# Kernel tuning notes

Hardware: AMD Instinct MI355X
Metric: run time of the kernel (lower is better)

Reference implementation:

```python
import jax, jax.numpy as jnp
import numpy as np

HIDDEN = 96
N_NODES = 50000
N_EDGES = 800000
IN_DIM = 256


def setup_inputs() -> dict:
    key = jax.random.key(0)
    ks = jax.random.split(key, 8)
    x = jax.random.normal(ks[0], (N_NODES, IN_DIM), dtype=jnp.float32)
    d = jax.random.uniform(ks[1], (N_NODES,), dtype=jnp.float32)
    src = jax.random.randint(ks[2], (N_EDGES,), 0, N_NODES, dtype=jnp.int32)
    dst = jax.random.randint(ks[3], (N_EDGES,), 0, N_NODES, dtype=jnp.int32)
    # Xavier-normal-ish init scaled like the torch module (gain 1.414)
    W_in = jax.random.normal(ks[4], (HIDDEN, IN_DIM), dtype=jnp.float32) * (1.414 * np.sqrt(2.0 / (HIDDEN + IN_DIM)))
    b_in = jnp.zeros((HIDDEN,), dtype=jnp.float32)
    W_gate = jax.random.normal(ks[5], (HIDDEN, 2 * HIDDEN), dtype=jnp.float32) * (1.414 * np.sqrt(2.0 / (3 * HIDDEN)))
    b_gate = jnp.zeros((HIDDEN,), dtype=jnp.float32)
    W_clf = jax.random.normal(ks[6], (2, HIDDEN), dtype=jnp.float32) * np.sqrt(2.0 / (2 + HIDDEN))
    b_clf = jnp.zeros((2,), dtype=jnp.float32)
    return {"x": x, "d": d, "src": src, "dst": dst,
            "W_in": W_in, "b_in": b_in, "W_gate": W_gate, "b_gate": b_gate,
            "W_clf": W_clf, "b_clf": b_clf}


def reference(x, d, src, dst, W_in, b_in, W_gate, b_gate, W_clf, b_clf):
    # h = input_gate(x)
    h = x @ W_in.T + b_in                                  # [N, H]
    # NOTE: the original loop reassigns the same h every iteration, so every
    # num_layer iteration produces identical (z, a); one pass is the exact math.
    h_src = h[src]                                         # [E, H] gather
    h_dst = h[dst]                                         # [E, H] gather
    h2 = jnp.concatenate([h_dst, h_src], axis=1)           # [E, 2H]
    a = jnp.tanh((h2 @ W_gate.T + b_gate) / np.sqrt(2.0 * HIDDEN))  # [E, H]
    e = d[dst] * d[src]                                    # [E]
    msg = h_src * a * e[:, None]                           # [E, H]
    z = jax.ops.segment_sum(msg, dst, num_segments=N_NODES)  # scatter-sum to dst
    z = jax.nn.log_softmax(z @ W_clf.T + b_clf, axis=-1)   # [N, 2]
    return (z, a)
```

## Files before the change

kernel.cpp:

```cpp
#include <hip/hip_runtime.h>
#include <math.h>

#define HIDDEN 96
#define NNODES 50000
#define NEDGES 800000
#define INDIM  256
#define RS 0.07216878364870323f

__global__ void repack_kernel(const float* __restrict__ Wg, const float* __restrict__ bg,
                              float* __restrict__ V, float* __restrict__ bias2) {
    int idx = blockIdx.x * 256 + threadIdx.x;
    if (idx < 192 * 96) {
        int j = idx / 96, k = idx % 96;
        float v = (j < 96) ? Wg[j * 192 + k] : Wg[(j - 96) * 192 + 96 + k];
        V[idx] = v * RS;
    }
    if (idx < 192) bias2[idx] = (idx < 96) ? bg[idx] * RS : 0.0f;
}

__global__ __launch_bounds__(256) void gemm_nt_bias(
    const float* __restrict__ A, const float* __restrict__ B,
    const float* __restrict__ bias, float* __restrict__ C,
    int M, int K, int ldc) {
    __shared__ float As[128][36];
    __shared__ float Bs[96][36];
    const int tid = threadIdx.x;
    const int m0 = blockIdx.x * 128;
    const int n0 = blockIdx.y * 96;
    const int te = tid >> 4;
    const int tc = tid & 15;
    const int ra = tid >> 3;
    const int ka = (tid & 7) * 4;

    float acc[8][6];
#pragma unroll
    for (int i = 0; i < 8; i++)
#pragma unroll
        for (int j = 0; j < 6; j++) acc[i][j] = 0.0f;

    for (int k0 = 0; k0 < K; k0 += 32) {
#pragma unroll
        for (int r = 0; r < 4; r++) {
            int row = m0 + ra + r * 32;
            float4 v = make_float4(0, 0, 0, 0);
            if (row < M) v = *(const float4*)&A[(size_t)row * K + k0 + ka];
            *(float4*)&As[ra + r * 32][ka] = v;
        }
#pragma unroll
        for (int r = 0; r < 3; r++) {
            int row = n0 + ra + r * 32;
            float4 v = *(const float4*)&B[(size_t)row * K + k0 + ka];
            *(float4*)&Bs[ra + r * 32][ka] = v;
        }
        __syncthreads();
#pragma unroll
        for (int k4 = 0; k4 < 32; k4 += 4) {
            float4 af[8], bf[6];
#pragma unroll
            for (int i = 0; i < 8; i++) af[i] = *(float4*)&As[8 * te + i][k4];
#pragma unroll
            for (int j = 0; j < 6; j++) bf[j] = *(float4*)&Bs[6 * tc + j][k4];
#pragma unroll
            for (int i = 0; i < 8; i++)
#pragma unroll
                for (int j = 0; j < 6; j++)
                    acc[i][j] += af[i].x * bf[j].x + af[i].y * bf[j].y +
                                 af[i].z * bf[j].z + af[i].w * bf[j].w;
        }
        __syncthreads();
    }
#pragma unroll
    for (int i = 0; i < 8; i++) {
        int row = m0 + 8 * te + i;
        if (row < M) {
#pragma unroll
            for (int j = 0; j < 6; j++) {
                int col = n0 + 6 * tc + j;
                C[(size_t)row * ldc + col] = acc[i][j] + bias[col];
            }
        }
    }
}

__global__ void hist_kernel(const int* __restrict__ dst, int* __restrict__ counts) {
    int i = blockIdx.x * 256 + threadIdx.x;
    if (i < NEDGES) atomicAdd(&counts[dst[i]], 1);
}

__global__ __launch_bounds__(512) void scan1_kernel(const int* __restrict__ counts,
                                                    int* __restrict__ offsets,
                                                    int* __restrict__ btot) {
    __shared__ int sh[512];
    int tid = threadIdx.x;
    int i = blockIdx.x * 512 + tid;
    int v = (i < NNODES) ? counts[i] : 0;
    sh[tid] = v;
    __syncthreads();
    for (int off = 1; off < 512; off <<= 1) {
        int tmp = 0;
        if (tid >= off) tmp = sh[tid - off];
        __syncthreads();
        if (tid >= off) sh[tid] += tmp;
        __syncthreads();
    }
    if (i < NNODES) offsets[i] = sh[tid] - v;
    if (tid == 511) btot[blockIdx.x] = sh[511];
}

__global__ __launch_bounds__(128) void scan2_kernel(int* __restrict__ btot, int nb) {
    __shared__ int sh[128];
    int tid = threadIdx.x;
    int v = (tid < nb) ? btot[tid] : 0;
    sh[tid] = v;
    __syncthreads();
    for (int off = 1; off < 128; off <<= 1) {
        int tmp = 0;
        if (tid >= off) tmp = sh[tid - off];
        __syncthreads();
        if (tid >= off) sh[tid] += tmp;
        __syncthreads();
    }
    if (tid < nb) btot[tid] = sh[tid] - v;
}

__global__ __launch_bounds__(512) void scan3_kernel(int* __restrict__ offsets,
                                                    const int* __restrict__ btot) {
    int i = blockIdx.x * 512 + threadIdx.x;
    if (i < NNODES) offsets[i] += btot[blockIdx.x];
    if (i == 0) offsets[NNODES] = NEDGES;
}

__global__ void scatter_kernel(const int* __restrict__ src, const int* __restrict__ dst,
                               const int* __restrict__ offsets, int* __restrict__ cursor,
                               int* __restrict__ eidx, int* __restrict__ esrc) {
    int e = blockIdx.x * 256 + threadIdx.x;
    if (e < NEDGES) {
        int t = dst[e];
        int pos = offsets[t] + atomicAdd(&cursor[t], 1);
        eidx[pos] = e;
        esrc[pos] = src[e];
    }
}

#define GPB 32
#define TPG 24
__global__ __launch_bounds__(768) void agg_kernel(
    const float* __restrict__ P, const float* __restrict__ h,
    const float* __restrict__ dvec, const int* __restrict__ offsets,
    const int* __restrict__ eidx, const int* __restrict__ esrc,
    const float* __restrict__ Wc, const float* __restrict__ bc,
    float* __restrict__ a_out, float* __restrict__ z_out) {
    __shared__ float red0[GPB * TPG];
    __shared__ float red1[GPB * TPG];
    const int t = threadIdx.x;
    const int g = t / TPG;
    const int c = t % TPG;
    const int node = blockIdx.x * GPB + g;
    float s0 = 0.0f, s1 = 0.0f;
    if (node < NNODES) {
        float4 pd = *(const float4*)&P[(size_t)node * 192 + 4 * c];
        float dt = dvec[node];
        int start = offsets[node], end = offsets[node + 1];
        float4 z4 = make_float4(0, 0, 0, 0);
        for (int i = start; i < end; i++) {
            int e = eidx[i];
            int s = esrc[i];
            float4 ps = *(const float4*)&P[(size_t)s * 192 + 96 + 4 * c];
            float4 hs = *(const float4*)&h[(size_t)s * 96 + 4 * c];
            float ee = dt * dvec[s];
            float4 a4;
            a4.x = tanhf(pd.x + ps.x);
            a4.y = tanhf(pd.y + ps.y);
            a4.z = tanhf(pd.z + ps.z);
            a4.w = tanhf(pd.w + ps.w);
            *(float4*)&a_out[(size_t)e * 96 + 4 * c] = a4;
            z4.x += hs.x * a4.x * ee;
            z4.y += hs.y * a4.y * ee;
            z4.z += hs.z * a4.z * ee;
            z4.w += hs.w * a4.w * ee;
        }
        float4 w0 = *(const float4*)&Wc[4 * c];
        float4 w1 = *(const float4*)&Wc[96 + 4 * c];
        s0 = z4.x * w0.x + z4.y * w0.y + z4.z * w0.z + z4.w * w0.w;
        s1 = z4.x * w1.x + z4.y * w1.y + z4.z * w1.z + z4.w * w1.w;
    }
    red0[t] = s0;
    red1[t] = s1;
    __syncthreads();
    if (c == 0 && node < NNODES) {
        float a0 = bc[0], a1 = bc[1];
#pragma unroll
        for (int k = 0; k < TPG; k++) { a0 += red0[t + k]; a1 += red1[t + k]; }
        float m = fmaxf(a0, a1);
        float lse = m + logf(expf(a0 - m) + expf(a1 - m));
        z_out[2 * node + 0] = a0 - lse;
        z_out[2 * node + 1] = a1 - lse;
    }
}

extern "C" void kernel_launch(void* const* d_in, const int* in_sizes, int n_in,
                              void* d_out, int out_size, void* d_ws, size_t ws_size,
                              hipStream_t stream) {
    const float* x    = (const float*)d_in[0];
    const float* dvec = (const float*)d_in[1];
    const int*   src  = (const int*)d_in[2];
    const int*   dst  = (const int*)d_in[3];
    const float* W_in = (const float*)d_in[4];
    const float* b_in = (const float*)d_in[5];
    const float* W_g  = (const float*)d_in[6];
    const float* b_g  = (const float*)d_in[7];
    const float* W_c  = (const float*)d_in[8];
    const float* b_c  = (const float*)d_in[9];

    float* z_out = (float*)d_out;
    float* a_out = (float*)d_out + 2 * NNODES;

    char* ws = (char*)d_ws;
    float* h       = (float*)(ws);
    float* P       = (float*)(ws + 19200000);
    float* V       = (float*)(ws + 57600000);
    float* b2      = (float*)(ws + 57673728);
    int*   offsets = (int*)  (ws + 57674752);
    int*   counts  = (int*)  (ws + 57874816);
    int*   cursor  = (int*)  (ws + 58074880);
    int*   btot    = (int*)  (ws + 58274944);
    int*   eidx    = (int*)  (ws + 58275456);
    int*   esrc    = (int*)  (ws + 61475456);

    hipMemsetAsync(counts, 0, NNODES * sizeof(int), stream);
    hipMemsetAsync(cursor, 0, NNODES * sizeof(int), stream);

    repack_kernel<<<dim3((192 * 96 + 255) / 256), 256, 0, stream>>>(W_g, b_g, V, b2);
    gemm_nt_bias<<<dim3((NNODES + 127) / 128, 1), 256, 0, stream>>>(x, W_in, b_in, h, NNODES, INDIM, HIDDEN);
    gemm_nt_bias<<<dim3((NNODES + 127) / 128, 2), 256, 0, stream>>>(h, V, b2, P, NNODES, HIDDEN, 192);

    const int NB = (NNODES + 511) / 512;
    hist_kernel<<<dim3((NEDGES + 255) / 256), 256, 0, stream>>>(dst, counts);
    scan1_kernel<<<dim3(NB), 512, 0, stream>>>(counts, offsets, btot);
    scan2_kernel<<<dim3(1), 128, 0, stream>>>(btot, NB);
    scan3_kernel<<<dim3(NB), 512, 0, stream>>>(offsets, btot);
    scatter_kernel<<<dim3((NEDGES + 255) / 256), 256, 0, stream>>>(src, dst, offsets, cursor, eidx, esrc);

    agg_kernel<<<dim3((NNODES + GPB - 1) / GPB), GPB * TPG, 0, stream>>>(
        P, h, dvec, offsets, eidx, esrc, W_c, b_c, a_out, z_out);
}
```

Baseline: 741.2 us.

## Pack edge records, fast tanh, nontemporal a stores, strided GEMM tiles, unroll aggregation

Several independent changes land together. The scatter step now writes packed int4 edge records (edge id, src, d[src]) and gets its cursor initialised by the scan, which removes a memset and the offset read. The aggregation kernel unrolls by two edges, uses an exp/rcp-based tanh, and writes the large `a` output with nontemporal stores to avoid polluting the cache. The GEMM register tile is remapped to a strided pattern to reduce LDS bank conflicts, and the aggregation block size is halved. The fast tanh trades some accuracy for speed.

```diff
diff --git a/kernel.cpp b/kernel.cpp
--- a/kernel.cpp
+++ b/kernel.cpp
@@ -6,6 +6,20 @@
 #define NEDGES 800000
 #define INDIM  256
 #define RS 0.07216878364870323f
+
+typedef float f4raw __attribute__((ext_vector_type(4)));
+
+__device__ __forceinline__ void nt_store4(float* p, float4 v) {
+    f4raw r;
+    r.x = v.x; r.y = v.y; r.z = v.z; r.w = v.w;
+    __builtin_nontemporal_store(r, (f4raw*)p);
+}
+
+__device__ __forceinline__ float fast_tanh(float x) {
+    x = fminf(15.0f, fmaxf(-15.0f, x));
+    float e = __expf(2.0f * x);
+    return (e - 1.0f) * __builtin_amdgcn_rcpf(e + 1.0f);
+}
 
 __global__ void repack_kernel(const float* __restrict__ Wg, const float* __restrict__ bg,
                               float* __restrict__ V, float* __restrict__ bias2) {
@@ -57,9 +71,9 @@
         for (int k4 = 0; k4 < 32; k4 += 4) {
             float4 af[8], bf[6];
 #pragma unroll
-            for (int i = 0; i < 8; i++) af[i] = *(float4*)&As[8 * te + i][k4];
-#pragma unroll
-            for (int j = 0; j < 6; j++) bf[j] = *(float4*)&Bs[6 * tc + j][k4];
+            for (int i = 0; i < 8; i++) af[i] = *(float4*)&As[te + 16 * i][k4];
+#pragma unroll
+            for (int j = 0; j < 6; j++) bf[j] = *(float4*)&Bs[tc + 16 * j][k4];
 #pragma unroll
             for (int i = 0; i < 8; i++)
 #pragma unroll
@@ -71,11 +85,11 @@
     }
 #pragma unroll
     for (int i = 0; i < 8; i++) {
-        int row = m0 + 8 * te + i;
+        int row = m0 + te + 16 * i;
         if (row < M) {
 #pragma unroll
             for (int j = 0; j < 6; j++) {
-                int col = n0 + 6 * tc + j;
+                int col = n0 + tc + 16 * j;
                 C[(size_t)row * ldc + col] = acc[i][j] + bias[col];
             }
         }
@@ -124,30 +138,35 @@
 }
 
 __global__ __launch_bounds__(512) void scan3_kernel(int* __restrict__ offsets,
+                                                    int* __restrict__ cursor,
                                                     const int* __restrict__ btot) {
     int i = blockIdx.x * 512 + threadIdx.x;
-    if (i < NNODES) offsets[i] += btot[blockIdx.x];
+    if (i < NNODES) {
+        int v = offsets[i] + btot[blockIdx.x];
+        offsets[i] = v;
+        cursor[i] = v;
+    }
     if (i == 0) offsets[NNODES] = NEDGES;
 }
 
 __global__ void scatter_kernel(const int* __restrict__ src, const int* __restrict__ dst,
-                               const int* __restrict__ offsets, int* __restrict__ cursor,
-                               int* __restrict__ eidx, int* __restrict__ esrc) {
+                               const float* __restrict__ dvec,
+                               int* __restrict__ cursor, int4* __restrict__ epack) {
     int e = blockIdx.x * 256 + threadIdx.x;
     if (e < NEDGES) {
         int t = dst[e];
-        int pos = offsets[t] + atomicAdd(&cursor[t], 1);
-        eidx[pos] = e;
-        esrc[pos] = src[e];
-    }
-}
-
-#define GPB 32
+        int s = src[e];
+        int pos = atomicAdd(&cursor[t], 1);
+        epack[pos] = make_int4(e, s, __float_as_int(dvec[s]), 0);
+    }
+}
+
+#define GPB 16
 #define TPG 24
-__global__ __launch_bounds__(768) void agg_kernel(
+__global__ __launch_bounds__(GPB * TPG) void agg_kernel(
     const float* __restrict__ P, const float* __restrict__ h,
     const float* __restrict__ dvec, const int* __restrict__ offsets,
-    const int* __restrict__ eidx, const int* __restrict__ esrc,
+    const int4* __restrict__ epack,
     const float* __restrict__ Wc, const float* __restrict__ bc,
     float* __restrict__ a_out, float* __restrict__ z_out) {
     __shared__ float red0[GPB * TPG];
@@ -160,24 +179,49 @@
     if (node < NNODES) {
         float4 pd = *(const float4*)&P[(size_t)node * 192 + 4 * c];
         float dt = dvec[node];
-        int start = offsets[node], end = offsets[node + 1];
+        int i = offsets[node];
+        const int end = offsets[node + 1];
         float4 z4 = make_float4(0, 0, 0, 0);
-        for (int i = start; i < end; i++) {
-            int e = eidx[i];
-            int s = esrc[i];
-            float4 ps = *(const float4*)&P[(size_t)s * 192 + 96 + 4 * c];
-            float4 hs = *(const float4*)&h[(size_t)s * 96 + 4 * c];
-            float ee = dt * dvec[s];
-            float4 a4;
-            a4.x = tanhf(pd.x + ps.x);
-            a4.y = tanhf(pd.y + ps.y);
-            a4.z = tanhf(pd.z + ps.z);
-            a4.w = tanhf(pd.w + ps.w);
-            *(float4*)&a_out[(size_t)e * 96 + 4 * c] = a4;
-            z4.x += hs.x * a4.x * ee;
-            z4.y += hs.y * a4.y * ee;
-            z4.z += hs.z * a4.z * ee;
-            z4.w += hs.w * a4.w * ee;
+        for (; i + 2 <= end; i += 2) {
+            int4 p0 = epack[i];
+            int4 p1 = epack[i + 1];
+            float4 ps0 = *(const float4*)&P[(size_t)p0.y * 192 + 96 + 4 * c];
+            float4 hs0 = *(const float4*)&h[(size_t)p0.y * 96 + 4 * c];
+            float4 ps1 = *(const float4*)&P[(size_t)p1.y * 192 + 96 + 4 * c];
+            float4 hs1 = *(const float4*)&h[(size_t)p1.y * 96 + 4 * c];
+            float e0 = dt * __int_as_float(p0.z);
+            float e1 = dt * __int_as_float(p1.z);
+            float4 a0, a1;
+            a0.x = fast_tanh(pd.x + ps0.x);
+            a0.y = fast_tanh(pd.y + ps0.y);
+            a0.z = fast_tanh(pd.z + ps0.z);
+            a0.w = fast_tanh(pd.w + ps0.w);
+            a1.x = fast_tanh(pd.x + ps1.x);
+            a1.y = fast_tanh(pd.y + ps1.y);
+            a1.z = fast_tanh(pd.z + ps1.z);
+            a1.w = fast_tanh(pd.w + ps1.w);
+            nt_store4(&a_out[(size_t)p0.x * 96 + 4 * c], a0);
+            nt_store4(&a_out[(size_t)p1.x * 96 + 4 * c], a1);
+            z4.x += hs0.x * a0.x * e0 + hs1.x * a1.x * e1;
+            z4.y += hs0.y * a0.y * e0 + hs1.y * a1.y * e1;
+            z4.z += hs0.z * a0.z * e0 + hs1.z * a1.z * e1;
+            z4.w += hs0.w * a0.w * e0 + hs1.w * a1.w * e1;
+        }
+        if (i < end) {
+            int4 p0 = epack[i];
+            float4 ps0 = *(const float4*)&P[(size_t)p0.y * 192 + 96 + 4 * c];
+            float4 hs0 = *(const float4*)&h[(size_t)p0.y * 96 + 4 * c];
+            float e0 = dt * __int_as_float(p0.z);
+            float4 a0;
+            a0.x = fast_tanh(pd.x + ps0.x);
+            a0.y = fast_tanh(pd.y + ps0.y);
+            a0.z = fast_tanh(pd.z + ps0.z);
+            a0.w = fast_tanh(pd.w + ps0.w);
+            nt_store4(&a_out[(size_t)p0.x * 96 + 4 * c], a0);
+            z4.x += hs0.x * a0.x * e0;
+            z4.y += hs0.y * a0.y * e0;
+            z4.z += hs0.z * a0.z * e0;
+            z4.w += hs0.w * a0.w * e0;
         }
         float4 w0 = *(const float4*)&Wc[4 * c];
         float4 w1 = *(const float4*)&Wc[96 + 4 * c];
@@ -224,11 +268,9 @@
     int*   counts  = (int*)  (ws + 57874816);
     int*   cursor  = (int*)  (ws + 58074880);
     int*   btot    = (int*)  (ws + 58274944);
-    int*   eidx    = (int*)  (ws + 58275456);
-    int*   esrc    = (int*)  (ws + 61475456);
-
-    hipMemsetAsync(counts, 0, NNODES * sizeof(int), stream);
-    hipMemsetAsync(cursor, 0, NNODES * sizeof(int), stream);
+    int4*  epack   = (int4*) (ws + 58275968);
+
+    (void)hipMemsetAsync(counts, 0, NNODES * sizeof(int), stream);
 
     repack_kernel<<<dim3((192 * 96 + 255) / 256), 256, 0, stream>>>(W_g, b_g, V, b2);
     gemm_nt_bias<<<dim3((NNODES + 127) / 128, 1), 256, 0, stream>>>(x, W_in, b_in, h, NNODES, INDIM, HIDDEN);
@@ -238,9 +280,9 @@
     hist_kernel<<<dim3((NEDGES + 255) / 256), 256, 0, stream>>>(dst, counts);
     scan1_kernel<<<dim3(NB), 512, 0, stream>>>(counts, offsets, btot);
     scan2_kernel<<<dim3(1), 128, 0, stream>>>(btot, NB);
-    scan3_kernel<<<dim3(NB), 512, 0, stream>>>(offsets, btot);
-    scatter_kernel<<<dim3((NEDGES + 255) / 256), 256, 0, stream>>>(src, dst, offsets, cursor, eidx, esrc);
+    scan3_kernel<<<dim3(NB), 512, 0, stream>>>(offsets, cursor, btot);
+    scatter_kernel<<<dim3((NEDGES + 255) / 256), 256, 0, stream>>>(src, dst, dvec, cursor, epack);
 
     agg_kernel<<<dim3((NNODES + GPB - 1) / GPB), GPB * TPG, 0, stream>>>(
-        P, h, dvec, offsets, eidx, esrc, W_c, b_c, a_out, z_out);
-}
+        P, h, dvec, offsets, epack, W_c, b_c, a_out, z_out);
+}
```

New measurement: 769.4 us. 1.04x slower.
